# Performance work log

Measured on AMD Instinct MI355X. Metric: run time of the kernel, lower is better.

Reference implementation:

```python
import jax, jax.numpy as jnp
import numpy as np

N = 50000

def gcn_conv(x, src, dst, W, b):
    # PyG GCNConv: h = x @ W; symmetric norm with self-loops; out = Ahat h + b
    h = x @ W  # [N, F]
    e = src.shape[0]
    deg = jax.ops.segment_sum(jnp.ones((e,), h.dtype), dst, num_segments=N) + 1.0  # +1 self-loop
    dinv = jax.lax.rsqrt(deg)  # deg >= 1 so finite
    norm = dinv[src] * dinv[dst]  # [E]
    agg = jax.ops.segment_sum(h[src] * norm[:, None], dst, num_segments=N)
    agg = agg + h * (dinv * dinv)[:, None]  # self-loop contribution
    return agg + b


def setup_inputs() -> dict:
    key = jax.random.key(0)
    ks = jax.random.split(key, 12)
    E = 400000
    x = jax.random.normal(ks[0], (N, 768), dtype=jnp.float32)
    edge_index = jax.random.randint(ks[1], (2, E), 0, N, dtype=jnp.int32)
    dims = [(768, 1536), (1536, 768), (768, 384), (384, 192), (192, 5)]
    inp = {"x": x, "edge_index": edge_index}
    for i, (fi, fo) in enumerate(dims):
        s = 1.0 / np.sqrt(fi)
        inp[f"W{i+1}"] = jax.random.uniform(ks[2 + 2 * i], (fi, fo), jnp.float32, -s, s)
        inp[f"b{i+1}"] = jnp.zeros((fo,), jnp.float32)
    return inp


def reference(x, edge_index, W1, b1, W2, b2, W3, b3, W4, b4, W5, b5):
    src, dst = edge_index[0], edge_index[1]
    h = x
    for W, b in [(W1, b1), (W2, b2), (W3, b3), (W4, b4)]:
        h = jax.nn.relu(gcn_conv(h, src, dst, W, b))
        # F.dropout with training=False is identity (eval mode)
    out = gcn_conv(h, src, dst, W5, b5)
    return (h, out)
```

## Files before the change

kernel.cpp:

```cpp
#include <hip/hip_runtime.h>
#include <stdint.h>

typedef unsigned short u16;
typedef unsigned int   u32;

#define NN 50000
#define NE 400000

typedef __bf16 bf16x8 __attribute__((ext_vector_type(8)));
typedef u16    u16x8  __attribute__((ext_vector_type(8)));
typedef u16    u16x4  __attribute__((ext_vector_type(4)));
typedef float  f32x4  __attribute__((ext_vector_type(4)));

__device__ __forceinline__ float bf2f(u16 b) {
  union { u32 u; float f; } v; v.u = ((u32)b) << 16; return v.f;
}
__device__ __forceinline__ u16 f2bf(float f) {
  union { float f; u32 u; } v; v.f = f;
  u32 r = v.u + 0x7fffu + ((v.u >> 16) & 1u);
  return (u16)(r >> 16);
}


__global__ void zero2_kernel(int* __restrict__ a, int* __restrict__ b, int n) {
  int i = blockIdx.x * blockDim.x + threadIdx.x;
  if (i < n) { a[i] = 0; b[i] = 0; }
}

__global__ void count_deg_kernel(const int* __restrict__ dst, int* __restrict__ deg, int e) {
  int i = blockIdx.x * blockDim.x + threadIdx.x;
  if (i < e) atomicAdd(&deg[dst[i]], 1);
}

__global__ void dinv_kernel(const int* __restrict__ deg, float* __restrict__ dinv, int n) {
  int i = blockIdx.x * blockDim.x + threadIdx.x;
  if (i < n) dinv[i] = rsqrtf((float)deg[i] + 1.0f);
}

__global__ __launch_bounds__(1024) void scan_kernel(const int* __restrict__ counts,
                                                    int* __restrict__ offsets, int n) {
  __shared__ int wsums[17];
  __shared__ int carry;
  int tid = threadIdx.x;
  int lane = tid & 63, wid = tid >> 6;
  if (tid == 0) carry = 0;
  __syncthreads();
  for (int base = 0; base < n; base += 1024) {
    int i = base + tid;
    int v = (i < n) ? counts[i] : 0;
    int s = v;
    #pragma unroll
    for (int off = 1; off < 64; off <<= 1) {
      int t = __shfl_up(s, off, 64);
      if (lane >= off) s += t;
    }
    if (lane == 63) wsums[wid] = s;
    __syncthreads();
    if (tid == 0) {
      int a = 0;
      #pragma unroll
      for (int w = 0; w < 16; ++w) { int t = wsums[w]; wsums[w] = a; a += t; }
      wsums[16] = a;
    }
    __syncthreads();
    if (i < n) offsets[i] = carry + wsums[wid] + s - v;
    __syncthreads();
    if (tid == 0) carry += wsums[16];
    __syncthreads();
  }
  if (tid == 0) offsets[n] = carry;
}

__global__ void csr_fill_kernel(const int* __restrict__ src, const int* __restrict__ dst,
                                const int* __restrict__ offsets, int* __restrict__ cursor,
                                const float* __restrict__ dinv,
                                int2* __restrict__ csr_pack, int e) {
  int i = blockIdx.x * blockDim.x + threadIdx.x;
  if (i < e) {
    int s = src[i], d = dst[i];
    int pos = offsets[d] + atomicAdd(&cursor[d], 1);
    float nr = dinv[s] * dinv[d];
    csr_pack[pos] = make_int2(s, __float_as_int(nr));
  }
}

__global__ void f2bf4_kernel(const float* __restrict__ in, u16* __restrict__ out, int n4) {
  int i = blockIdx.x * blockDim.x + threadIdx.x;
  if (i < n4) {
    f32x4 v = *(const f32x4*)(in + (size_t)i * 4);
    u16x4 o;
    #pragma unroll
    for (int k = 0; k < 4; ++k) o[k] = f2bf(v[k]);
    *(u16x4*)(out + (size_t)i * 4) = o;
  }
}

__device__ __forceinline__ void wt_one(const float* W, u16* Wt, int i, int K, int N) {
  int k = i / N;
  int n2 = i - k * N;
  Wt[n2 * K + k] = f2bf(W[i]);
}

#define WT_O1 1179648
#define WT_O2 2359296
#define WT_O3 2654208
#define WT_O4 2727936
#define WT_O5 2728896
__global__ void wt_all_kernel(const float* __restrict__ W1, u16* __restrict__ W1t,
                              const float* __restrict__ W2, u16* __restrict__ W2t,
                              const float* __restrict__ W3, u16* __restrict__ W3t,
                              const float* __restrict__ W4, u16* __restrict__ W4t,
                              const float* __restrict__ W5, u16* __restrict__ W5t) {
  int i = blockIdx.x * blockDim.x + threadIdx.x;
  if (i < WT_O1)      wt_one(W1, W1t, i, 768, 1536);
  else if (i < WT_O2) wt_one(W2, W2t, i - WT_O1, 1536, 768);
  else if (i < WT_O3) wt_one(W3, W3t, i - WT_O2, 768, 384);
  else if (i < WT_O4) wt_one(W4, W4t, i - WT_O3, 384, 192);
  else if (i < WT_O5) wt_one(W5, W5t, i - WT_O4, 192, 5);
}


template<int G, bool HAS_BIAS, bool RELU, bool OUT_BF, bool OUT_F32>
__global__ __launch_bounds__(256) void agg8_kernel(
    const u16* __restrict__ g, const int* __restrict__ rowptr,
    const int2* __restrict__ csr_pack,
    const float* __restrict__ dinv, const float* __restrict__ bias,
    u16* __restrict__ outb, float* __restrict__ outf)
{
  constexpr int F = G * 8;
  int idx = blockIdx.x * blockDim.x + threadIdx.x;
  if (idx >= NN * G) return;
  int v = idx / G;
  int g8 = idx - v * G;
  const u16* base = g + g8 * 8;

  float acc[8];
  #pragma unroll
  for (int k = 0; k < 8; ++k) acc[k] = 0.f;

  int e0 = rowptr[v], e1 = rowptr[v + 1];
  int e = e0;
  for (; e + 3 < e1; e += 4) {
    int2 p0 = csr_pack[e];
    int2 p1 = csr_pack[e + 1];
    int2 p2 = csr_pack[e + 2];
    int2 p3 = csr_pack[e + 3];
    u16x8 r0 = *(const u16x8*)(base + (size_t)p0.x * F);
    u16x8 r1 = *(const u16x8*)(base + (size_t)p1.x * F);
    u16x8 r2 = *(const u16x8*)(base + (size_t)p2.x * F);
    u16x8 r3 = *(const u16x8*)(base + (size_t)p3.x * F);
    float n0 = __int_as_float(p0.y), n1 = __int_as_float(p1.y);
    float n2 = __int_as_float(p2.y), n3 = __int_as_float(p3.y);
    #pragma unroll
    for (int k = 0; k < 8; ++k) acc[k] += n0 * bf2f(r0[k]);
    #pragma unroll
    for (int k = 0; k < 8; ++k) acc[k] += n1 * bf2f(r1[k]);
    #pragma unroll
    for (int k = 0; k < 8; ++k) acc[k] += n2 * bf2f(r2[k]);
    #pragma unroll
    for (int k = 0; k < 8; ++k) acc[k] += n3 * bf2f(r3[k]);
  }
  for (; e < e1; ++e) {
    int2 p0 = csr_pack[e];
    u16x8 r0 = *(const u16x8*)(base + (size_t)p0.x * F);
    float n0 = __int_as_float(p0.y);
    #pragma unroll
    for (int k = 0; k < 8; ++k) acc[k] += n0 * bf2f(r0[k]);
  }

  float sv = dinv[v]; sv *= sv;
  u16x8 sr = *(const u16x8*)(base + (size_t)v * F);
  float vals[8];
  #pragma unroll
  for (int k = 0; k < 8; ++k) {
    float val = acc[k] + sv * bf2f(sr[k]);
    if (HAS_BIAS) val += bias[g8 * 8 + k];
    if (RELU) val = fmaxf(val, 0.f);
    vals[k] = val;
  }
  if (OUT_BF) {
    u16x8 ob;
    #pragma unroll
    for (int k = 0; k < 8; ++k) ob[k] = f2bf(vals[k]);
    *(u16x8*)(outb + (size_t)v * F + g8 * 8) = ob;
  }
  if (OUT_F32) {
    f32x4 o0, o1;
    #pragma unroll
    for (int k = 0; k < 4; ++k) { o0[k] = vals[k]; o1[k] = vals[4 + k]; }
    float* op = outf + (size_t)v * F + g8 * 8;
    *(f32x4*)op = o0;
    *(f32x4*)(op + 4) = o1;
  }
}

__global__ void agg_small_kernel(const u16* __restrict__ g, const int* __restrict__ rowptr,
                                 const int2* __restrict__ csr_pack,
                                 const float* __restrict__ dinv, const float* __restrict__ bias,
                                 float* __restrict__ out, int n, int F) {
  int idx = blockIdx.x * blockDim.x + threadIdx.x;
  if (idx >= n * F) return;
  int v = idx / F;
  int f = idx - v * F;
  float acc = 0.f;
  int e1 = rowptr[v + 1];
  for (int e = rowptr[v]; e < e1; ++e) {
    int2 p = csr_pack[e];
    acc += __int_as_float(p.y) * bf2f(g[p.x * F + f]);
  }
  float dv = dinv[v];
  out[idx] = acc + dv * dv * bf2f(g[v * F + f]) + bias[f];
}


#define BM 128
#define BN 128
#define BK 32

#define WAIT_VMCNT4 0x0F74
#define WAIT_VMCNT0 0x0F70

__device__ __forceinline__ void gl_lds16(const void* g, void* l) {
  __builtin_amdgcn_global_load_lds((const __attribute__((address_space(1))) void*)g,
                                   (__attribute__((address_space(3))) void*)l, 16, 0, 0);
}

template<bool BIAS_RELU>
__global__ __launch_bounds__(256, 4) void gemm_bt_kernel(
    const u16* __restrict__ A, const u16* __restrict__ Bt,
    u16* __restrict__ C, const float* __restrict__ bias,
    int M, int N, int K)
{
  __shared__ __align__(16) u16 As[2][BM * BK];
  __shared__ __align__(16) u16 Bs[2][BN * BK];
  int gm = (M + BM - 1) / BM;
  int gn = (N + BN - 1) / BN;
  int bid = blockIdx.x;
  int xcd = bid & 7;
  int t = bid >> 3;
  int trow = t / gn;
  int bn_i = t - trow * gn;
  int row = trow * 8 + xcd;
  if (row >= gm) return;
  int bm = row * BM, bn = bn_i * BN;

  int tid = threadIdx.x;
  int wave = tid >> 6, lane = tid & 63;
  int wm = wave & 1, wn = wave >> 1;

  int srow = tid >> 2;
  int sq_log = ((tid & 3) - ((tid >> 3) & 3)) & 3;
  int ar0 = min(bm + srow, M - 1);
  int ar1 = min(bm + 64 + srow, M - 1);
  int br0 = min(bn + srow, N - 1);
  int br1 = min(bn + 64 + srow, N - 1);
  const u16* ag0 = A + (size_t)ar0 * K + sq_log * 8;
  const u16* ag1 = A + (size_t)ar1 * K + sq_log * 8;
  const u16* bg0 = Bt + (size_t)br0 * K + sq_log * 8;
  const u16* bg1 = Bt + (size_t)br1 * K + sq_log * 8;
  int la0 = (wave * 16) * BK;
  int la1 = (64 + wave * 16) * BK;

  f32x4 acc[4][4];
  #pragma unroll
  for (int i = 0; i < 4; ++i)
    #pragma unroll
    for (int j = 0; j < 4; ++j)
      acc[i][j] = (f32x4){0.f, 0.f, 0.f, 0.f};

  int row16 = lane & 15, q = lane >> 4;
  int perm = (q + (row16 >> 1)) & 3;
  int ard = (wm * 64 + row16) * BK + perm * 8;
  int brd = (wn * 64 + row16) * BK + perm * 8;

  const int iters = K / BK;

  gl_lds16(ag0, &As[0][la0]);
  gl_lds16(ag1, &As[0][la1]);
  gl_lds16(bg0, &Bs[0][la0]);
  gl_lds16(bg1, &Bs[0][la1]);

  int buf = 0;
  for (int it = 0; it < iters; ++it) {
    __builtin_amdgcn_s_barrier();
    if (it + 1 < iters) {
      int kn = (it + 1) * BK;
      gl_lds16(ag0 + kn, &As[buf ^ 1][la0]);
      gl_lds16(ag1 + kn, &As[buf ^ 1][la1]);
      gl_lds16(bg0 + kn, &Bs[buf ^ 1][la0]);
      gl_lds16(bg1 + kn, &Bs[buf ^ 1][la1]);
      __builtin_amdgcn_s_waitcnt(WAIT_VMCNT4);
    } else {
      __builtin_amdgcn_s_waitcnt(WAIT_VMCNT0);
    }
    __builtin_amdgcn_s_barrier();

    bf16x8 af[4], bfr[4];
    #pragma unroll
    for (int i = 0; i < 4; ++i) af[i] = *(const bf16x8*)(&As[buf][ard + i * 16 * BK]);
    #pragma unroll
    for (int j = 0; j < 4; ++j) bfr[j] = *(const bf16x8*)(&Bs[buf][brd + j * 16 * BK]);
    #pragma unroll
    for (int i = 0; i < 4; ++i)
      #pragma unroll
      for (int j = 0; j < 4; ++j)
        acc[i][j] = __builtin_amdgcn_mfma_f32_16x16x32_bf16(af[i], bfr[j], acc[i][j], 0, 0, 0);
    buf ^= 1;
  }

  #pragma unroll
  for (int i = 0; i < 4; ++i) {
    int rbase = bm + wm * 64 + i * 16 + q * 4;
    #pragma unroll
    for (int j = 0; j < 4; ++j) {
      int col = bn + wn * 64 + j * 16 + row16;
      if (col < N) {
        float bv = BIAS_RELU ? bias[col] : 0.f;
        #pragma unroll
        for (int r = 0; r < 4; ++r) {
          int gr = rbase + r;
          if (gr < M) {
            float val = acc[i][j][r];
            if (BIAS_RELU) { val += bv; val = fmaxf(val, 0.f); }
            C[(size_t)gr * N + col] = f2bf(val);
          }
        }
      }
    }
  }
}

static inline int gemm_grid(int M, int N) {
  int gm = (M + BM - 1) / BM;
  int gn = (N + BN - 1) / BN;
  int rows_per_xcd = (gm + 7) / 8;
  return rows_per_xcd * gn * 8;
}


extern "C" void kernel_launch(void* const* d_in, const int* in_sizes, int n_in,
                              void* d_out, int out_size, void* d_ws, size_t ws_size,
                              hipStream_t stream) {
  const float* x   = (const float*)d_in[0];
  const int* ei    = (const int*)d_in[1];
  const int* src   = ei;
  const int* dst   = ei + NE;
  const float* W1  = (const float*)d_in[2];
  const float* b1  = (const float*)d_in[3];
  const float* W2  = (const float*)d_in[4];
  const float* b2  = (const float*)d_in[5];
  const float* W3  = (const float*)d_in[6];
  const float* b3  = (const float*)d_in[7];
  const float* W4  = (const float*)d_in[8];
  const float* b4  = (const float*)d_in[9];
  const float* W5  = (const float*)d_in[10];
  const float* b5  = (const float*)d_in[11];
  float* out_h = (float*)d_out;
  float* out_o = (float*)d_out + (size_t)NN * 192;

  char* p = (char*)d_ws;
  auto alloc = [&](size_t bytes) { char* r = p; p += (bytes + 255) & ~(size_t)255; return r; };
  int*   deg      = (int*)alloc((size_t)NN * 4);
  int*   cursor   = (int*)alloc((size_t)NN * 4);
  float* dinv     = (float*)alloc((size_t)NN * 4);
  int*   offs     = (int*)alloc((size_t)(NN + 1) * 4);
  int2*  csr_pack = (int2*)alloc((size_t)NE * 8);
  u16* W1t = (u16*)alloc((size_t)768 * 1536 * 2);
  u16* W2t = (u16*)alloc((size_t)1536 * 768 * 2);
  u16* W3t = (u16*)alloc((size_t)768 * 384 * 2);
  u16* W4t = (u16*)alloc((size_t)384 * 192 * 2);
  u16* W5t = (u16*)alloc((size_t)192 * 5 * 2);
  u16* B0 = (u16*)alloc((size_t)NN * 768 * 2);
  u16* B1 = (u16*)alloc((size_t)NN * 768 * 2);
  u16* B2 = (u16*)alloc((size_t)NN * 1536 * 2);

  u16* xb  = B0;
  u16* a0  = B1;
  u16* h1  = B2;
  u16* g2  = B0;
  u16* h2  = B1;
  u16* g3  = B0;
  u16* h3  = B2;
  u16* g4  = B0;
  u16* h4b = B1;
  u16* g5  = B0;

  const int M = NN;

  zero2_kernel<<<(NN + 255) / 256, 256, 0, stream>>>(deg, cursor, NN);
  count_deg_kernel<<<(NE + 255) / 256, 256, 0, stream>>>(dst, deg, NE);
  dinv_kernel<<<(NN + 255) / 256, 256, 0, stream>>>(deg, dinv, NN);
  scan_kernel<<<1, 1024, 0, stream>>>(deg, offs, NN);
  csr_fill_kernel<<<(NE + 255) / 256, 256, 0, stream>>>(src, dst, offs, cursor, dinv,
                                                        csr_pack, NE);
  f2bf4_kernel<<<((NN * 768 / 4) + 255) / 256, 256, 0, stream>>>(x, xb, NN * 768 / 4);
  wt_all_kernel<<<(WT_O5 + 255) / 256, 256, 0, stream>>>(W1, W1t, W2, W2t, W3, W3t,
                                                         W4, W4t, W5, W5t);

  dim3 blk(256);

  agg8_kernel<96, false, false, true, false><<<(NN * 96 + 255) / 256, blk, 0, stream>>>(
      xb, offs, csr_pack, dinv, nullptr, a0, nullptr);
  gemm_bt_kernel<true><<<gemm_grid(M, 1536), blk, 0, stream>>>(
      a0, W1t, h1, b1, M, 1536, 768);

  gemm_bt_kernel<false><<<gemm_grid(M, 768), blk, 0, stream>>>(
      h1, W2t, g2, nullptr, M, 768, 1536);
  agg8_kernel<96, true, true, true, false><<<(NN * 96 + 255) / 256, blk, 0, stream>>>(
      g2, offs, csr_pack, dinv, b2, h2, nullptr);

  gemm_bt_kernel<false><<<gemm_grid(M, 384), blk, 0, stream>>>(
      h2, W3t, g3, nullptr, M, 384, 768);
  agg8_kernel<48, true, true, true, false><<<(NN * 48 + 255) / 256, blk, 0, stream>>>(
      g3, offs, csr_pack, dinv, b3, h3, nullptr);

  gemm_bt_kernel<false><<<gemm_grid(M, 192), blk, 0, stream>>>(
      h3, W4t, g4, nullptr, M, 192, 384);
  agg8_kernel<24, true, true, true, true><<<(NN * 24 + 255) / 256, blk, 0, stream>>>(
      g4, offs, csr_pack, dinv, b4, h4b, out_h);

  gemm_bt_kernel<false><<<gemm_grid(M, 5), blk, 0, stream>>>(
      h4b, W5t, g5, nullptr, M, 5, 192);
  agg_small_kernel<<<((NN * 5) + 255) / 256, 256, 0, stream>>>(
      g5, offs, csr_pack, dinv, b5, out_o, NN, 5);
}
```

Baseline: 1.047 ms.

## Parallelize CSR offset scan and process two feature chunks per aggregation thread

Replaces the single-block serial prefix scan over node degrees with a three-kernel multi-block scan (block sums, scan of block sums, per-block local scan). Adds an agg16 aggregation kernel in which each thread handles two 8-wide feature chunks, halving thread count and the redundant CSR index/norm loads per feature for the 768-wide layers. The wider kernel raises per-thread register use and lowers occupancy, and the scan now costs two extra launches.

```diff
diff --git a/kernel.cpp b/kernel.cpp
--- a/kernel.cpp
+++ b/kernel.cpp
@@ -37,38 +37,66 @@
   if (i < n) dinv[i] = rsqrtf((float)deg[i] + 1.0f);
 }
 
-__global__ __launch_bounds__(1024) void scan_kernel(const int* __restrict__ counts,
-                                                    int* __restrict__ offsets, int n) {
-  __shared__ int wsums[17];
-  __shared__ int carry;
+__global__ void scan_part1(const int* __restrict__ counts, int* __restrict__ bsum, int n) {
+  __shared__ int ws[4];
   int tid = threadIdx.x;
+  int i = blockIdx.x * 256 + tid;
+  int v = (i < n) ? counts[i] : 0;
+  int s = v;
+  #pragma unroll
+  for (int off = 1; off < 64; off <<= 1) s += __shfl_xor(s, off, 64);
   int lane = tid & 63, wid = tid >> 6;
-  if (tid == 0) carry = 0;
+  if (lane == 0) ws[wid] = s;
   __syncthreads();
-  for (int base = 0; base < n; base += 1024) {
-    int i = base + tid;
-    int v = (i < n) ? counts[i] : 0;
-    int s = v;
-    #pragma unroll
-    for (int off = 1; off < 64; off <<= 1) {
-      int t = __shfl_up(s, off, 64);
-      if (lane >= off) s += t;
-    }
-    if (lane == 63) wsums[wid] = s;
-    __syncthreads();
-    if (tid == 0) {
-      int a = 0;
-      #pragma unroll
-      for (int w = 0; w < 16; ++w) { int t = wsums[w]; wsums[w] = a; a += t; }
-      wsums[16] = a;
-    }
-    __syncthreads();
-    if (i < n) offsets[i] = carry + wsums[wid] + s - v;
-    __syncthreads();
-    if (tid == 0) carry += wsums[16];
-    __syncthreads();
-  }
-  if (tid == 0) offsets[n] = carry;
+  if (tid == 0) bsum[blockIdx.x] = ws[0] + ws[1] + ws[2] + ws[3];
+}
+__global__ void scan_part2(int* __restrict__ bsum, int* __restrict__ totp, int nb) {
+  __shared__ int ws[5];
+  int tid = threadIdx.x;
+  int v = (tid < nb) ? bsum[tid] : 0;
+  int lane = tid & 63, wid = tid >> 6;
+  int s = v;
+  #pragma unroll
+  for (int off = 1; off < 64; off <<= 1) {
+    int t = __shfl_up(s, off, 64);
+    if (lane >= off) s += t;
+  }
+  if (lane == 63) ws[wid] = s;
+  __syncthreads();
+  if (tid == 0) {
+    int a = 0;
+    #pragma unroll
+    for (int w = 0; w < 4; ++w) { int t = ws[w]; ws[w] = a; a += t; }
+    ws[4] = a;
+  }
+  __syncthreads();
+  int ex = ws[wid] + s - v;
+  if (tid < nb) bsum[tid] = ex;
+  if (tid == 0) *totp = ws[4];
+}
+__global__ void scan_part3(const int* __restrict__ counts, const int* __restrict__ bsum,
+                           int* __restrict__ offsets, int n) {
+  __shared__ int ws[5];
+  int tid = threadIdx.x;
+  int i = blockIdx.x * 256 + tid;
+  int v = (i < n) ? counts[i] : 0;
+  int lane = tid & 63, wid = tid >> 6;
+  int s = v;
+  #pragma unroll
+  for (int off = 1; off < 64; off <<= 1) {
+    int t = __shfl_up(s, off, 64);
+    if (lane >= off) s += t;
+  }
+  if (lane == 63) ws[wid] = s;
+  __syncthreads();
+  if (tid == 0) {
+    int a = 0;
+    #pragma unroll
+    for (int w = 0; w < 4; ++w) { int t = ws[w]; ws[w] = a; a += t; }
+  }
+  __syncthreads();
+  int ex = ws[wid] + s - v;
+  if (i < n) offsets[i] = bsum[blockIdx.x] + ex;
 }
 
 __global__ void csr_fill_kernel(const int* __restrict__ src, const int* __restrict__ dst,
@@ -119,6 +147,76 @@
   else if (i < WT_O5) wt_one(W5, W5t, i - WT_O4, 192, 5);
 }
 
+
+template<int G2, bool HAS_BIAS, bool RELU>
+__global__ __launch_bounds__(256) void agg16_kernel(
+    const u16* __restrict__ g, const int* __restrict__ rowptr,
+    const int2* __restrict__ csr_pack,
+    const float* __restrict__ dinv, const float* __restrict__ bias,
+    u16* __restrict__ outb)
+{
+  constexpr int F = G2 * 16;
+  int idx = blockIdx.x * blockDim.x + threadIdx.x;
+  if (idx >= NN * G2) return;
+  int v = idx / G2;
+  int t = idx - v * G2;
+  const u16* base0 = g + t * 8;
+  const u16* base1 = g + (t + G2) * 8;
+
+  float acc0[8], acc1[8];
+  #pragma unroll
+  for (int k = 0; k < 8; ++k) { acc0[k] = 0.f; acc1[k] = 0.f; }
+
+  int e0 = rowptr[v], e1 = rowptr[v + 1];
+  int e = e0;
+  for (; e + 3 < e1; e += 4) {
+    int2 p0 = csr_pack[e];
+    int2 p1 = csr_pack[e + 1];
+    int2 p2 = csr_pack[e + 2];
+    int2 p3 = csr_pack[e + 3];
+    u16x8 a0 = *(const u16x8*)(base0 + (size_t)p0.x * F);
+    u16x8 b0 = *(const u16x8*)(base1 + (size_t)p0.x * F);
+    u16x8 a1 = *(const u16x8*)(base0 + (size_t)p1.x * F);
+    u16x8 b1 = *(const u16x8*)(base1 + (size_t)p1.x * F);
+    u16x8 a2 = *(const u16x8*)(base0 + (size_t)p2.x * F);
+    u16x8 b2 = *(const u16x8*)(base1 + (size_t)p2.x * F);
+    u16x8 a3 = *(const u16x8*)(base0 + (size_t)p3.x * F);
+    u16x8 b3 = *(const u16x8*)(base1 + (size_t)p3.x * F);
+    float n0 = __int_as_float(p0.y), n1 = __int_as_float(p1.y);
+    float n2 = __int_as_float(p2.y), n3 = __int_as_float(p3.y);
+    #pragma unroll
+    for (int k = 0; k < 8; ++k) { acc0[k] += n0 * bf2f(a0[k]); acc1[k] += n0 * bf2f(b0[k]); }
+    #pragma unroll
+    for (int k = 0; k < 8; ++k) { acc0[k] += n1 * bf2f(a1[k]); acc1[k] += n1 * bf2f(b1[k]); }
+    #pragma unroll
+    for (int k = 0; k < 8; ++k) { acc0[k] += n2 * bf2f(a2[k]); acc1[k] += n2 * bf2f(b2[k]); }
+    #pragma unroll
+    for (int k = 0; k < 8; ++k) { acc0[k] += n3 * bf2f(a3[k]); acc1[k] += n3 * bf2f(b3[k]); }
+  }
+  for (; e < e1; ++e) {
+    int2 p0 = csr_pack[e];
+    u16x8 a0 = *(const u16x8*)(base0 + (size_t)p0.x * F);
+    u16x8 b0 = *(const u16x8*)(base1 + (size_t)p0.x * F);
+    float n0 = __int_as_float(p0.y);
+    #pragma unroll
+    for (int k = 0; k < 8; ++k) { acc0[k] += n0 * bf2f(a0[k]); acc1[k] += n0 * bf2f(b0[k]); }
+  }
+
+  float sv = dinv[v]; sv *= sv;
+  u16x8 s0 = *(const u16x8*)(base0 + (size_t)v * F);
+  u16x8 s1 = *(const u16x8*)(base1 + (size_t)v * F);
+  u16x8 o0, o1;
+  #pragma unroll
+  for (int k = 0; k < 8; ++k) {
+    float v0 = acc0[k] + sv * bf2f(s0[k]);
+    float v1 = acc1[k] + sv * bf2f(s1[k]);
+    if (HAS_BIAS) { v0 += bias[t * 8 + k]; v1 += bias[(t + G2) * 8 + k]; }
+    if (RELU) { v0 = fmaxf(v0, 0.f); v1 = fmaxf(v1, 0.f); }
+    o0[k] = f2bf(v0); o1[k] = f2bf(v1);
+  }
+  *(u16x8*)(outb + (size_t)v * F + t * 8) = o0;
+  *(u16x8*)(outb + (size_t)v * F + (t + G2) * 8) = o1;
+}
 
 template<int G, bool HAS_BIAS, bool RELU, bool OUT_BF, bool OUT_F32>
 __global__ __launch_bounds__(256) void agg8_kernel(
@@ -364,6 +462,7 @@
   int*   cursor   = (int*)alloc((size_t)NN * 4);
   float* dinv     = (float*)alloc((size_t)NN * 4);
   int*   offs     = (int*)alloc((size_t)(NN + 1) * 4);
+  int*   bsum     = (int*)alloc((size_t)256 * 4);
   int2*  csr_pack = (int2*)alloc((size_t)NE * 8);
   u16* W1t = (u16*)alloc((size_t)768 * 1536 * 2);
   u16* W2t = (u16*)alloc((size_t)1536 * 768 * 2);
@@ -386,11 +485,14 @@
   u16* g5  = B0;
 
   const int M = NN;
-
-  zero2_kernel<<<(NN + 255) / 256, 256, 0, stream>>>(deg, cursor, NN);
+  const int NBLK = (NN + 255) / 256;
+
+  zero2_kernel<<<NBLK, 256, 0, stream>>>(deg, cursor, NN);
   count_deg_kernel<<<(NE + 255) / 256, 256, 0, stream>>>(dst, deg, NE);
-  dinv_kernel<<<(NN + 255) / 256, 256, 0, stream>>>(deg, dinv, NN);
-  scan_kernel<<<1, 1024, 0, stream>>>(deg, offs, NN);
+  dinv_kernel<<<NBLK, 256, 0, stream>>>(deg, dinv, NN);
+  scan_part1<<<NBLK, 256, 0, stream>>>(deg, bsum, NN);
+  scan_part2<<<1, 256, 0, stream>>>(bsum, offs + NN, NBLK);
+  scan_part3<<<NBLK, 256, 0, stream>>>(deg, bsum, offs, NN);
   csr_fill_kernel<<<(NE + 255) / 256, 256, 0, stream>>>(src, dst, offs, cursor, dinv,
                                                         csr_pack, NE);
   f2bf4_kernel<<<((NN * 768 / 4) + 255) / 256, 256, 0, stream>>>(x, xb, NN * 768 / 4);
@@ -399,15 +501,15 @@
 
   dim3 blk(256);
 
-  agg8_kernel<96, false, false, true, false><<<(NN * 96 + 255) / 256, blk, 0, stream>>>(
-      xb, offs, csr_pack, dinv, nullptr, a0, nullptr);
+  agg16_kernel<48, false, false><<<(NN * 48 + 255) / 256, blk, 0, stream>>>(
+      xb, offs, csr_pack, dinv, nullptr, a0);
   gemm_bt_kernel<true><<<gemm_grid(M, 1536), blk, 0, stream>>>(
       a0, W1t, h1, b1, M, 1536, 768);
 
   gemm_bt_kernel<false><<<gemm_grid(M, 768), blk, 0, stream>>>(
       h1, W2t, g2, nullptr, M, 768, 1536);
-  agg8_kernel<96, true, true, true, false><<<(NN * 96 + 255) / 256, blk, 0, stream>>>(
-      g2, offs, csr_pack, dinv, b2, h2, nullptr);
+  agg16_kernel<48, true, true><<<(NN * 48 + 255) / 256, blk, 0, stream>>>(
+      g2, offs, csr_pack, dinv, b2, h2);
 
   gemm_bt_kernel<false><<<gemm_grid(M, 384), blk, 0, stream>>>(
       h2, W3t, g3, nullptr, M, 384, 768);
```

Result: faster. 1.017 ms (-2.8%).
